# Kernel optimization log

Hardware: AMD Instinct MI355X
Metric: run time of the kernel (lower is better)

## Reference

```python
import jax, jax.numpy as jnp
import numpy as np

N, E, B = 20000, 60000, 800
H = 64          # node_out_feats
EOUT = 64       # edge_out_feats
D = H + EOUT    # set2set input dim = 128
NT = 138        # n_tasks


def _forward(node_feats, edge_feats, fp_vector, src, dst, gid,
             Wn, bn, We1, be1, We2, be2, Wres, Wgx, bgx, Wgh, bgh,
             Wep, bep,
             Wlx0, Wlh0, bl0, Wlx1, Wlh1, bl1, Wlx2, Wlh2, bl2,
             Wfp, bfp, bn_g, bn_b, bn_m, bn_v,
             Wf1, bf1, Wf2, bf2, Wp, bp):
    # ---- CustomMPNNGNN (dgllife MPNNGNN: proj + NNConv(edge-net) + GRU) ----
    h = jax.nn.relu(node_feats @ Wn + bn)                       # [N,64]
    We = jax.nn.relu(edge_feats @ We1 + be1) @ We2 + be2        # [E,4096]
    We = We.reshape(-1, H, H)                                   # [E,64,64] per-edge weight
    hs = h                                                      # GRU hidden state
    for _ in range(3):
        msg = jnp.einsum('ei,eio->eo', h[src], We)              # edge gather + matvec
        agg = jax.ops.segment_sum(msg, dst, num_segments=N)     # scatter-add to dst
        m = jax.nn.relu(agg + h @ Wres)                         # residual root weight
        gx = m @ Wgx + bgx
        gh = hs @ Wgh + bgh
        xr, xz, xn = jnp.split(gx, 3, axis=-1)
        hr, hz, hn = jnp.split(gh, 3, axis=-1)
        r = jax.nn.sigmoid(xr + hr)
        z = jax.nn.sigmoid(xz + hz)
        n = jnp.tanh(xn + r * hn)
        hs = (1.0 - z) * n + z * hs
        h = hs
    # ---- _internal_readout: gather src node emb + projected edge emb, segment-sum at dst ----
    e_emb = jax.nn.relu(edge_feats @ Wep + bep)                 # [E,64]
    src_msg = jnp.concatenate([h[src], e_emb], axis=1)          # [E,128]
    feat = jax.ops.segment_sum(src_msg, dst, num_segments=N)    # [N,128]
    # ---- Set2Set (3-layer LSTM hidden 128, 6 iterations) ----
    q_star = jnp.zeros((B, 2 * D), feat.dtype)
    hc = [(jnp.zeros((B, D), feat.dtype), jnp.zeros((B, D), feat.dtype)) for _ in range(3)]
    lstm = [(Wlx0, Wlh0, bl0), (Wlx1, Wlh1, bl1), (Wlx2, Wlh2, bl2)]
    for _ in range(6):
        x = q_star
        new_hc = []
        for (Wx, Wh, b), (hl, cl) in zip(lstm, hc):
            g = x @ Wx + hl @ Wh + b                            # [B,512] gates i,f,g,o
            gi, gf, gg, go = jnp.split(g, 4, axis=-1)
            cl = jax.nn.sigmoid(gf) * cl + jax.nn.sigmoid(gi) * jnp.tanh(gg)
            hl = jax.nn.sigmoid(go) * jnp.tanh(cl)
            new_hc.append((hl, cl))
            x = hl
        hc = new_hc
        q = x                                                   # [B,128]
        e = jnp.sum(feat * q[gid], axis=-1)                     # [N]
        emax = jax.ops.segment_max(e, gid, num_segments=B)
        a = jnp.exp(e - emax[gid])
        denom = jax.ops.segment_sum(a, gid, num_segments=B)
        alpha = a / (denom[gid] + 1e-9)
        r = jax.ops.segment_sum(alpha[:, None] * feat, gid, num_segments=B)  # [B,128]
        q_star = jnp.concatenate([q, r], axis=1)                # [B,256]
    # ---- Fingerprint encoder: Linear + BatchNorm1d(eval) + ReLU ----
    fp = fp_vector @ Wfp + bfp
    fp = jax.nn.relu((fp - bn_m) * bn_g * jax.lax.rsqrt(bn_v + 1e-5) + bn_b)  # [B,128]
    # ---- combined FFN (384 -> 300 -> 256) + prediction head ----
    comb = jnp.concatenate([q_star, fp], axis=1)                # [B,384]
    emb = jax.nn.relu(comb @ Wf1 + bf1) @ Wf2 + bf2             # [B,256]
    out = jax.nn.relu(emb) @ Wp + bp                            # [B,138]
    return out


def setup_inputs() -> dict:
    key = jax.random.key(0)
    ks = iter(jax.random.split(key, 64))
    def nrm(shape, s):
        return jax.random.normal(next(ks), shape, jnp.float32) * s
    inp = {}
    inp['node_feats'] = jax.random.normal(next(ks), (N, 134), jnp.float32)
    inp['edge_feats'] = jax.random.uniform(next(ks), (E, 6), jnp.float32)
    inp['fp_vector'] = jax.random.uniform(next(ks), (B, 1024), jnp.float32)
    inp['src'] = jax.random.randint(next(ks), (E,), 0, N)
    inp['dst'] = jax.random.randint(next(ks), (E,), 0, N)
    inp['gid'] = jnp.sort(jax.random.randint(next(ks), (N,), 0, B))
    # MPNN params
    inp['Wn'] = nrm((134, H), 0.08); inp['bn'] = jnp.zeros((H,), jnp.float32)
    inp['We1'] = nrm((6, 128), 0.2); inp['be1'] = jnp.zeros((128,), jnp.float32)
    inp['We2'] = nrm((128, H * H), 0.05); inp['be2'] = jnp.zeros((H * H,), jnp.float32)
    inp['Wres'] = nrm((H, H), 0.1)
    inp['Wgx'] = nrm((H, 3 * H), 0.1); inp['bgx'] = jnp.zeros((3 * H,), jnp.float32)
    inp['Wgh'] = nrm((H, 3 * H), 0.1); inp['bgh'] = jnp.zeros((3 * H,), jnp.float32)
    # edge projection for readout
    inp['Wep'] = nrm((6, EOUT), 0.2); inp['bep'] = jnp.zeros((EOUT,), jnp.float32)
    # Set2Set LSTM (layer0 input 2D=256, layers 1-2 input D=128, hidden D=128)
    inp['Wlx0'] = nrm((2 * D, 4 * D), 0.06); inp['Wlh0'] = nrm((D, 4 * D), 0.06); inp['bl0'] = jnp.zeros((4 * D,), jnp.float32)
    inp['Wlx1'] = nrm((D, 4 * D), 0.06); inp['Wlh1'] = nrm((D, 4 * D), 0.06); inp['bl1'] = jnp.zeros((4 * D,), jnp.float32)
    inp['Wlx2'] = nrm((D, 4 * D), 0.06); inp['Wlh2'] = nrm((D, 4 * D), 0.06); inp['bl2'] = jnp.zeros((4 * D,), jnp.float32)
    # fingerprint encoder
    inp['Wfp'] = nrm((1024, 128), 0.03); inp['bfp'] = jnp.zeros((128,), jnp.float32)
    inp['bn_g'] = jnp.ones((128,), jnp.float32); inp['bn_b'] = jnp.zeros((128,), jnp.float32)
    inp['bn_m'] = jnp.zeros((128,), jnp.float32); inp['bn_v'] = jnp.ones((128,), jnp.float32)
    # combined FFN + prediction head
    inp['Wf1'] = nrm((2 * D + 128, 300), 0.06); inp['bf1'] = jnp.zeros((300,), jnp.float32)
    inp['Wf2'] = nrm((300, 256), 0.06); inp['bf2'] = jnp.zeros((256,), jnp.float32)
    inp['Wp'] = nrm((256, NT), 0.06); inp['bp'] = jnp.zeros((NT,), jnp.float32)
    return inp


def reference(node_feats, edge_feats, fp_vector, src, dst, gid,
              Wn, bn, We1, be1, We2, be2, Wres, Wgx, bgx, Wgh, bgh,
              Wep, bep,
              Wlx0, Wlh0, bl0, Wlx1, Wlh1, bl1, Wlx2, Wlh2, bl2,
              Wfp, bfp, bn_g, bn_b, bn_m, bn_v,
              Wf1, bf1, Wf2, bf2, Wp, bp):
    return _forward(node_feats, edge_feats, fp_vector, src, dst, gid,
                    Wn, bn, We1, be1, We2, be2, Wres, Wgx, bgx, Wgh, bgh,
                    Wep, bep,
                    Wlx0, Wlh0, bl0, Wlx1, Wlh1, bl1, Wlx2, Wlh2, bl2,
                    Wfp, bfp, bn_g, bn_b, bn_m, bn_v,
                    Wf1, bf1, Wf2, bf2, Wp, bp)
```

## Files before the change

kernel.cpp:

```cpp
#include <hip/hip_runtime.h>

typedef short short8 __attribute__((ext_vector_type(8)));
typedef float f32x4  __attribute__((ext_vector_type(4)));

#define NN 20000
#define NE 60000
#define NB 800
#define NTASK 138
#define EB 128

#define O_WX0 0
#define O_WH0 131072
#define O_WX1 196608
#define O_WH1 262144
#define O_WX2 327680
#define O_WH2 393216
#define O_WF1 458752
#define O_WF2 573952
#define O_WP  650752
#define NWB   686080

static __device__ __forceinline__ float sigm(float x) { return 1.f / (1.f + expf(-x)); }

static __device__ __forceinline__ unsigned short f2bf(float x) {
    unsigned u = __float_as_uint(x);
    unsigned r = (u + 0x7fffu + ((u >> 16) & 1u)) >> 16;
    return (unsigned short)r;
}
static __device__ __forceinline__ float bf2f(unsigned short b) {
    return __uint_as_float(((unsigned)b) << 16);
}

__global__ void kpre(float* __restrict__ zbase, int nz4,
                     const float* __restrict__ We2, const float* __restrict__ be2,
                     unsigned short* __restrict__ thi,
                     const int* __restrict__ gid, int* __restrict__ seg,
                     const float* __restrict__ fpv, const float* __restrict__ Wfp,
                     const float* __restrict__ bfpv,
                     const float* __restrict__ bng, const float* __restrict__ bnb,
                     const float* __restrict__ bnm, const float* __restrict__ bnv,
                     float* __restrict__ fpb,
                     const float* __restrict__ nf, const float* __restrict__ Wn,
                     const float* __restrict__ bn, float* __restrict__ hf,
                     unsigned short* __restrict__ hb,
                     const float* __restrict__ Wlx0, const float* __restrict__ Wlh0,
                     const float* __restrict__ Wlx1, const float* __restrict__ Wlh1,
                     const float* __restrict__ Wlx2, const float* __restrict__ Wlh2,
                     const float* __restrict__ Wf1, const float* __restrict__ Wf2,
                     const float* __restrict__ Wp, unsigned short* __restrict__ wb,
                     int B0, int B1, int B2, int B3, int B4) {
    __shared__ float st[64 * 65];
    __shared__ float sNF[16 * 134];
    __shared__ float sred[128];
    const int bid = blockIdx.x, tid = threadIdx.x;
    if (bid < B0) {
        long base = (long)bid * 2048 + tid;
        #pragma unroll
        for (int r = 0; r < 8; ++r) {
            long i = base + r * 256;
            if (i < nz4) reinterpret_cast<f32x4*>(zbase)[i] = f32x4{0.f, 0.f, 0.f, 0.f};
        }
    } else if (bid < B1) {
        int c = bid - B0;
        const float* srcp = (c < 128) ? We2 + (long)c * 4096 : be2;
        for (int idx = tid; idx < 4096; idx += 256) {
            int o = idx & 63, i = idx >> 6;
            st[o * 65 + i] = srcp[idx];
        }
        __syncthreads();
        for (int idx = tid; idx < 4096; idx += 256) {
            int i = idx & 63, o = idx >> 6;
            thi[(long)c * 4096 + idx] = f2bf(st[o * 65 + i]);
        }
    } else if (bid < B2) {
        int b = (bid - B1) * 256 + tid;
        if (b <= NB) {
            int lo = 0, hi = NN;
            while (lo < hi) { int mid = (lo + hi) >> 1; if (gid[mid] < b) lo = mid + 1; else hi = mid; }
            seg[b] = lo;
        }
    } else if (bid < B3) {
        int g = bid - B2;
        int u = tid & 127, half = tid >> 7;
        float acc = half ? 0.f : bfpv[u];
        const float* fr = fpv + (long)g * 1024 + half * 512;
        const float* wr = Wfp + (long)half * 512 * 128;
        for (int k = 0; k < 512; ++k) acc += fr[k] * wr[k * 128 + u];
        if (half) sred[u] = acc;
        __syncthreads();
        if (!half) {
            acc += sred[u];
            float sc = bng[u] / sqrtf(bnv[u] + 1e-5f);
            fpb[(long)g * 128 + u] = fmaxf((acc - bnm[u]) * sc + bnb[u], 0.f);
        }
    } else if (bid < B4) {
        int n0 = (bid - B3) * 16;
        const float* nfb = nf + (long)n0 * 134;
        for (int i = tid; i < 16 * 134; i += 256) sNF[i] = nfb[i];
        __syncthreads();
        int u = tid & 63, jg = tid >> 6;
        float a[4];
        float bv = bn[u];
        #pragma unroll
        for (int jj = 0; jj < 4; ++jj) a[jj] = bv;
        for (int k = 0; k < 134; ++k) {
            float w = Wn[k * 64 + u];
            #pragma unroll
            for (int jj = 0; jj < 4; ++jj) a[jj] += sNF[(jg * 4 + jj) * 134 + k] * w;
        }
        #pragma unroll
        for (int jj = 0; jj < 4; ++jj) {
            long o = (long)(n0 + jg * 4 + jj) * 64 + u;
            float v = fmaxf(a[jj], 0.f);
            hf[o] = v;
            hb[o] = f2bf(v);
        }
    } else {
        int t0 = (bid - B4) * 2048 + tid;
        #pragma unroll
        for (int r = 0; r < 8; ++r) {
            int i = t0 + r * 256;
            if (i >= NWB) break;
            float v;
            if (i < O_WF1) {
                const float* srcp; int base;
                if (i < O_WH0)      { srcp = Wlx0; base = O_WX0; }
                else if (i < O_WX1) { srcp = Wlh0; base = O_WH0; }
                else if (i < O_WH1) { srcp = Wlx1; base = O_WX1; }
                else if (i < O_WX2) { srcp = Wlh1; base = O_WH1; }
                else if (i < O_WH2) { srcp = Wlx2; base = O_WX2; }
                else                { srcp = Wlh2; base = O_WH2; }
                int il = i - base;
                int kb = il >> 12, g = (il >> 3) & 511, kk = il & 7;
                v = srcp[(kb * 8 + kk) * 512 + g];
            }
            else if (i < O_WF2) v = Wf1[i - O_WF1];
            else if (i < O_WP)  v = Wf2[i - O_WF2];
            else                v = Wp[i - O_WP];
            wb[i] = f2bf(v);
        }
    }
}

__global__ __launch_bounds__(256) void keinsum(
    const unsigned short* __restrict__ hb,
    const float* __restrict__ hf, const float* __restrict__ Wres,
    const float* __restrict__ ef, const float* __restrict__ We1, const float* __restrict__ be1,
    const unsigned short* __restrict__ thi,
    const int* __restrict__ src, const int* __restrict__ dst,
    float* __restrict__ agg) {
    __shared__ __align__(16) unsigned short sB[3 * 64 * 72];
    __shared__ __align__(16) float sX[3 * EB];
    __shared__ float sEF[6 * EB];
    const int bid = blockIdx.x, tid = threadIdx.x;
    if (bid >= 469) {
        int t = (bid - 469) * 256 + tid;
        int u = t & 63;
        int n0 = (t >> 6) * 8;
        if (n0 >= NN) return;
        float a[8] = {0.f, 0.f, 0.f, 0.f, 0.f, 0.f, 0.f, 0.f};
        for (int k = 0; k < 64; ++k) {
            float w = Wres[k * 64 + u];
            #pragma unroll
            for (int j = 0; j < 8; ++j) a[j] += hf[(long)(n0 + j) * 64 + k] * w;
        }
        #pragma unroll
        for (int j = 0; j < 8; ++j) atomicAdd(&agg[(long)(n0 + j) * 64 + u], a[j]);
        return;
    }
    const int lane = tid & 63, wave = tid >> 6;
    const int m = lane & 15, q = lane >> 4;
    const int eb = bid * EB;
    const int ew = (wave >> 1) * 64;
    const int e0 = eb + ew;
    const int nt0 = (wave & 1) * 2;
    const int c0 = 0, c1 = 129;

    for (int i = tid; i < 6 * EB; i += 256) {
        int e = i / 6, k = i % 6;
        int ee = eb + e; if (ee >= NE) ee = NE - 1;
        sEF[k * EB + e] = ef[(long)ee * 6 + k];
    }

    short8 ahi[4][2];
    #pragma unroll
    for (int eg = 0; eg < 4; ++eg) {
        int em = e0 + eg * 16 + m; if (em >= NE) em = NE - 1;
        int sn = src[em];
        ahi[eg][0] = *reinterpret_cast<const short8*>(hb + (long)sn * 64 + q * 8);
        ahi[eg][1] = *reinterpret_cast<const short8*>(hb + (long)sn * 64 + 32 + q * 8);
    }
    float msg[4][2][4];
    #pragma unroll
    for (int eg = 0; eg < 4; ++eg)
        #pragma unroll
        for (int nt = 0; nt < 2; ++nt)
            #pragma unroll
            for (int r = 0; r < 4; ++r) msg[eg][nt][r] = 0.f;

    short8 rB[2][2];
    auto GLOAD = [&](int c, int setv) {
        const unsigned short* bb = thi + (long)c * 4096;
        #pragma unroll
        for (int it = 0; it < 2; ++it) {
            int u = tid + it * 256;
            rB[setv][it] = *reinterpret_cast<const short8*>(bb + u * 8);
        }
    };
    auto DSW = [&](int buf, int setv, int c) {
        unsigned short* base = &sB[buf * 4608];
        #pragma unroll
        for (int it = 0; it < 2; ++it) {
            int u = tid + it * 256;
            *reinterpret_cast<short8*>(&base[(u >> 3) * 72 + (u & 7) * 8]) = rB[setv][it];
        }
        if (tid < EB) {
            float xv = 1.f;
            if (c < 128) {
                float a = be1[c];
                #pragma unroll
                for (int k = 0; k < 6; ++k) a += sEF[k * EB + tid] * We1[k * 128 + c];
                xv = fmaxf(a, 0.f);
            }
            sX[buf * EB + tid] = xv;
        }
    };
    auto CMP = [&](int buf) {
        const unsigned short* base = &sB[buf * 4608];
        f32x4 xw[4];
        #pragma unroll
        for (int eg = 0; eg < 4; ++eg)
            xw[eg] = *reinterpret_cast<const f32x4*>(&sX[buf * EB + ew + eg * 16 + q * 4]);
        short8 b0[2], b1[2];
        #pragma unroll
        for (int nt = 0; nt < 2; ++nt) {
            const unsigned short* rp = &base[((nt0 + nt) * 16 + m) * 72 + q * 8];
            b0[nt] = *reinterpret_cast<const short8*>(rp);
            b1[nt] = *reinterpret_cast<const short8*>(rp + 32);
        }
        #pragma unroll
        for (int eg = 0; eg < 4; ++eg)
            #pragma unroll
            for (int nt = 0; nt < 2; ++nt) {
                f32x4 z = {0.f, 0.f, 0.f, 0.f};
                z = __builtin_amdgcn_mfma_f32_16x16x32_bf16(ahi[eg][0], b0[nt], z, 0, 0, 0);
                z = __builtin_amdgcn_mfma_f32_16x16x32_bf16(ahi[eg][1], b1[nt], z, 0, 0, 0);
                #pragma unroll
                for (int r = 0; r < 4; ++r) msg[eg][nt][r] += xw[eg][r] * z[r];
            }
    };

    GLOAD(c0, 0);
    GLOAD(c0 + 1, 1);
    __syncthreads();
    DSW(0, 0, c0);
    int c = c0;
    for (; c + 1 < c1; c += 2) {
        int s = (c - c0) % 3;
        if (c + 2 < c1) GLOAD(c + 2, 0);
        __syncthreads();
        DSW((s + 1) % 3, 1, c + 1);
        CMP(s);
        if (c + 3 < c1) GLOAD(c + 3, 1);
        __syncthreads();
        if (c + 2 < c1) DSW((s + 2) % 3, 0, c + 2);
        CMP((s + 1) % 3);
    }
    if (c < c1) { __syncthreads(); CMP((c - c0) % 3); }

    #pragma unroll
    for (int eg = 0; eg < 4; ++eg)
        #pragma unroll
        for (int r = 0; r < 4; ++r) {
            int e = e0 + eg * 16 + q * 4 + r;
            if (e < NE) {
                int d = dst[e];
                #pragma unroll
                for (int nt = 0; nt < 2; ++nt)
                    atomicAdd(&agg[(long)d * 64 + (nt0 + nt) * 16 + m], msg[eg][nt][r]);
            }
        }
}

__global__ void kgruz(const float* __restrict__ agg, const float* __restrict__ h,
                      const float* __restrict__ Wgx, const float* __restrict__ bgx,
                      const float* __restrict__ Wgh, const float* __restrict__ bgh,
                      float* __restrict__ hof, unsigned short* __restrict__ hb,
                      float* __restrict__ aggN) {
    const int bid = blockIdx.x, tid = threadIdx.x;
    if (bid >= 625) {
        long base = (long)(bid - 625) * 2048 + tid;
        #pragma unroll
        for (int r = 0; r < 8; ++r) {
            long i = base + r * 256;
            if (i < 320000) reinterpret_cast<f32x4*>(aggN)[i] = f32x4{0.f, 0.f, 0.f, 0.f};
        }
        return;
    }
    __shared__ float sA[2048], sH[2048];
    const int n0 = bid * 32;
    const float* ab = agg + (long)n0 * 64;
    const float* hrow = h + (long)n0 * 64;
    for (int i = tid; i < 2048; i += 256) { sA[i] = ab[i]; sH[i] = hrow[i]; }
    __syncthreads();
    const int u = tid & 63, jg = tid >> 6;
    float xr[8], xz[8], xn[8], hr[8], hz[8], hn[8];
    float b0 = bgx[u], b1 = bgx[64 + u], b2 = bgx[128 + u];
    float d0 = bgh[u], d1 = bgh[64 + u], d2 = bgh[128 + u];
    #pragma unroll
    for (int j = 0; j < 8; ++j) {
        xr[j] = b0; xz[j] = b1; xn[j] = b2;
        hr[j] = d0; hz[j] = d1; hn[j] = d2;
    }
    for (int k = 0; k < 64; ++k) {
        float w0 = Wgx[k * 192 + u], w1 = Wgx[k * 192 + 64 + u], w2 = Wgx[k * 192 + 128 + u];
        float v0 = Wgh[k * 192 + u], v1 = Wgh[k * 192 + 64 + u], v2 = Wgh[k * 192 + 128 + u];
        #pragma unroll
        for (int j = 0; j < 8; ++j) {
            int n = jg * 8 + j;
            float mk = fmaxf(sA[n * 64 + k], 0.f);
            float hk = sH[n * 64 + k];
            xr[j] += mk * w0; xz[j] += mk * w1; xn[j] += mk * w2;
            hr[j] += hk * v0; hz[j] += hk * v1; hn[j] += hk * v2;
        }
    }
    #pragma unroll
    for (int j = 0; j < 8; ++j) {
        int n = jg * 8 + j;
        float rg = sigm(xr[j] + hr[j]);
        float zg = sigm(xz[j] + hz[j]);
        float ng = tanhf(xn[j] + rg * hn[j]);
        long o = (long)(n0 + n) * 64 + u;
        float hv = (1.f - zg) * ng + zg * sH[n * 64 + u];
        hof[o] = hv;
        hb[o] = f2bf(hv);
    }
}

__global__ void kreadout(const float* __restrict__ h,
                         const float* __restrict__ ef, const float* __restrict__ Wep,
                         const float* __restrict__ bep,
                         const int* __restrict__ src, const int* __restrict__ dst,
                         float* __restrict__ feat) {
    int t = blockIdx.x * blockDim.x + threadIdx.x;
    if (t >= NE * 128) return;
    int e = t >> 7, j = t & 127;
    float v;
    if (j < 64) {
        v = h[(long)src[e] * 64 + j];
    } else {
        int o = j - 64;
        v = bep[o];
        #pragma unroll
        for (int k = 0; k < 6; ++k) v += ef[(long)e * 6 + k] * Wep[k * 64 + o];
        v = fmaxf(v, 0.f);
    }
    atomicAdd(&feat[(long)dst[e] * 128 + j], v);
}

__global__ __launch_bounds__(512) void klstmattn(
    const float* __restrict__ qstar_in, float* __restrict__ qstar_out,
    const float* __restrict__ feat, const int* __restrict__ seg,
    float* __restrict__ esg,
    const unsigned short* __restrict__ wb,
    const float* __restrict__ bl0, const float* __restrict__ bl1, const float* __restrict__ bl2,
    const float* __restrict__ h0i, const float* __restrict__ c0i, float* __restrict__ h0o, float* __restrict__ c0o,
    const float* __restrict__ h1i, const float* __restrict__ c1i, float* __restrict__ h1o, float* __restrict__ c1o,
    const float* __restrict__ h2i, const float* __restrict__ c2i, float* __restrict__ h2o, float* __restrict__ c2o,
    const float* __restrict__ fpb,
    const float* __restrict__ bf1, const float* __restrict__ bf2, const float* __restrict__ bp,
    float* __restrict__ out, int do_head) {
    __shared__ float sXH[2][256];
    __shared__ float sHin[2][128];
    __shared__ float sG[2][512];
    __shared__ float sE[2][512];
    __shared__ float sH2[2][128];
    __shared__ float sR[2][2][128];
    __shared__ float sred[2][4];
    __shared__ float s1b[2][300];
    __shared__ float s2[2][256];
    const int tid = threadIdx.x;
    const int b0g = blockIdx.x * 2;
    const unsigned short* Wx[3] = {wb + O_WX0, wb + O_WX1, wb + O_WX2};
    const unsigned short* Wh[3] = {wb + O_WH0, wb + O_WH1, wb + O_WH2};
    const float* bl[3] = {bl0, bl1, bl2};
    const float* hin[3] = {h0i, h1i, h2i};
    const float* cin[3] = {c0i, c1i, c2i};
    float* hout[3] = {h0o, h1o, h2o};
    float* cout[3] = {c0o, c1o, c2o};

    {
        int b = tid >> 8, u = tid & 255;
        sXH[b][u] = qstar_in[(long)(b0g + b) * 256 + u];
        if (tid < 256) {
            int bb = tid >> 7, uu = tid & 127;
            sHin[bb][uu] = h0i[(long)(b0g + bb) * 128 + uu];
        }
    }
    __syncthreads();

    for (int l = 0; l < 3; ++l) {
        const int Kx = l ? 128 : 256;
        const int g = tid;
        const unsigned short* wxp = Wx[l];
        const unsigned short* whp = Wh[l];
        float bv = bl[l][g];
        float a0 = bv, a1 = bv, a0b = 0.f, a1b = 0.f;
        #pragma unroll 2
        for (int kb = 0; kb < (Kx >> 3); ++kb) {
            short8 wv = *reinterpret_cast<const short8*>(wxp + ((kb << 9) + g) * 8);
            const f32x4* xp0 = reinterpret_cast<const f32x4*>(&sXH[0][kb << 3]);
            const f32x4* xp1 = reinterpret_cast<const f32x4*>(&sXH[1][kb << 3]);
            f32x4 xa0 = xp0[0], xb0 = xp0[1];
            f32x4 xa1 = xp1[0], xb1 = xp1[1];
            #pragma unroll
            for (int kk = 0; kk < 4; ++kk) {
                float w0 = bf2f((unsigned short)wv[kk]);
                float w1 = bf2f((unsigned short)wv[kk + 4]);
                a0  += xa0[kk] * w0;  a1  += xa1[kk] * w0;
                a0b += xb0[kk] * w1;  a1b += xb1[kk] * w1;
            }
        }
        #pragma unroll 2
        for (int kb = 0; kb < 16; ++kb) {
            short8 wv = *reinterpret_cast<const short8*>(whp + ((kb << 9) + g) * 8);
            const f32x4* hp0 = reinterpret_cast<const f32x4*>(&sHin[0][kb << 3]);
            const f32x4* hp1 = reinterpret_cast<const f32x4*>(&sHin[1][kb << 3]);
            f32x4 ha0 = hp0[0], hb0 = hp0[1];
            f32x4 ha1 = hp1[0], hb1 = hp1[1];
            #pragma unroll
            for (int kk = 0; kk < 4; ++kk) {
                float w0 = bf2f((unsigned short)wv[kk]);
                float w1 = bf2f((unsigned short)wv[kk + 4]);
                a0  += ha0[kk] * w0;  a1  += ha1[kk] * w0;
                a0b += hb0[kk] * w1;  a1b += hb1[kk] * w1;
            }
        }
        sG[0][g] = a0 + a0b;
        sG[1][g] = a1 + a1b;
        __syncthreads();
        if (tid < 256) {
            int b = tid >> 7, u = tid & 127;
            float gi = sG[b][u], gf = sG[b][128 + u], gg = sG[b][256 + u], go = sG[b][384 + u];
            long idx = (long)(b0g + b) * 128 + u;
            float c_ = sigm(gf) * cin[l][idx] + sigm(gi) * tanhf(gg);
            float h_ = sigm(go) * tanhf(c_);
            cout[l][idx] = c_;
            hout[l][idx] = h_;
            sXH[b][u] = h_;
            if (l == 2) sH2[b][u] = h_;
        } else if (l < 2) {
            int t2 = tid - 256;
            int b = t2 >> 7, u = t2 & 127;
            sHin[b][u] = hin[l + 1][(long)(b0g + b) * 128 + u];
        }
        __syncthreads();
    }

    const int group = tid >> 8;
    const int t = tid & 255;
    const int s0 = seg[b0g + group], s1 = seg[b0g + group + 1], len = s1 - s0;
    const int wv = t >> 6, lane = t & 63;
    for (int idx = wv; idx < len; idx += 4) {
        long n = s0 + idx;
        float p = feat[n * 128 + lane] * sH2[group][lane]
                + feat[n * 128 + 64 + lane] * sH2[group][64 + lane];
        for (int off = 32; off; off >>= 1) p += __shfl_down(p, off, 64);
        if (lane == 0) { if (idx < 512) sE[group][idx] = p; else esg[n] = p; }
    }
    __syncthreads();
    auto ev = [&](int i) { return i < 512 ? sE[group][i] : esg[s0 + i]; };
    float lm = -1e30f;
    for (int i = t; i < len; i += 256) lm = fmaxf(lm, ev(i));
    for (int off = 32; off; off >>= 1) lm = fmaxf(lm, __shfl_down(lm, off, 64));
    if (lane == 0) sred[group][wv] = lm;
    __syncthreads();
    float mx = fmaxf(fmaxf(sred[group][0], sred[group][1]),
                     fmaxf(sred[group][2], sred[group][3]));
    __syncthreads();
    float ls = 0.f;
    for (int i = t; i < len; i += 256) {
        float e_ = expf(ev(i) - mx);
        if (i < 512) sE[group][i] = e_; else esg[s0 + i] = e_;
        ls += e_;
    }
    for (int off = 32; off; off >>= 1) ls += __shfl_down(ls, off, 64);
    if (lane == 0) sred[group][wv] = ls;
    __syncthreads();
    float inv = 1.f / (sred[group][0] + sred[group][1] + sred[group][2] + sred[group][3] + 1e-9f);
    const int j = t & 127, half = t >> 7;
    float racc = 0.f;
    for (int i = half; i < len; i += 2)
        racc += ev(i) * feat[(long)(s0 + i) * 128 + j];
    sR[group][half][j] = racc;
    __syncthreads();
    float rr = (sR[group][0][j] + sR[group][1][j]) * inv;
    if (half == 0) {
        qstar_out[(long)(b0g + group) * 256 + j] = sH2[group][j];
        qstar_out[(long)(b0g + group) * 256 + 128 + j] = rr;
    }

    if (!do_head) return;
    __syncthreads();
    if (half == 0) {
        sE[group][j] = sH2[group][j];
        sE[group][128 + j] = rr;
    } else {
        sE[group][256 + j] = fpb[(long)(b0g + group) * 128 + j];
    }
    __syncthreads();
    const unsigned short* Wf1b = wb + O_WF1;
    const unsigned short* Wf2b = wb + O_WF2;
    const unsigned short* Wpb  = wb + O_WP;
    for (int task = tid; task < 600; task += 512) {
        int g = task / 300, u = task % 300;
        float acc = bf1[u];
        for (int k = 0; k < 384; ++k) acc += sE[g][k] * bf2f(Wf1b[k * 300 + u]);
        s1b[g][u] = fmaxf(acc, 0.f);
    }
    __syncthreads();
    for (int task = tid; task < 512; task += 512) {
        int g = task >> 8, u = task & 255;
        float acc = bf2[u];
        for (int k = 0; k < 300; ++k) acc += s1b[g][k] * bf2f(Wf2b[k * 256 + u]);
        s2[g][u] = fmaxf(acc, 0.f);
    }
    __syncthreads();
    for (int task = tid; task < 2 * NTASK; task += 512) {
        int g = task / NTASK, u = task % NTASK;
        float acc = bp[u];
        for (int k = 0; k < 256; ++k) acc += s2[g][k] * bf2f(Wpb[k * NTASK + u]);
        out[(long)(b0g + g) * NTASK + u] = acc;
    }
}

extern "C" void kernel_launch(void* const* d_in, const int* in_sizes, int n_in,
                              void* d_out, int out_size, void* d_ws, size_t ws_size,
                              hipStream_t stream) {
    auto fp_ = [&](int i) { return (const float*)d_in[i]; };
    auto ip_ = [&](int i) { return (const int*)d_in[i]; };
    const float *nf = fp_(0), *ef = fp_(1), *fpv = fp_(2);
    const int *src = ip_(3), *dst = ip_(4), *gid = ip_(5);
    const float *Wn = fp_(6), *bn = fp_(7), *We1 = fp_(8), *be1 = fp_(9);
    const float *We2 = fp_(10), *be2 = fp_(11), *Wres = fp_(12);
    const float *Wgx = fp_(13), *bgx = fp_(14), *Wgh = fp_(15), *bgh = fp_(16);
    const float *Wep = fp_(17), *bep = fp_(18);
    const float *Wlx0 = fp_(19), *Wlh0 = fp_(20), *bl0 = fp_(21);
    const float *Wlx1 = fp_(22), *Wlh1 = fp_(23), *bl1 = fp_(24);
    const float *Wlx2 = fp_(25), *Wlh2 = fp_(26), *bl2 = fp_(27);
    const float *Wfp = fp_(28), *bfpv = fp_(29);
    const float *bng = fp_(30), *bnb = fp_(31), *bnm = fp_(32), *bnv = fp_(33);
    const float *Wf1 = fp_(34), *bf1 = fp_(35), *Wf2 = fp_(36), *bf2 = fp_(37);
    const float *Wp = fp_(38), *bp = fp_(39);

    char* w = (char*)d_ws;
    auto alloc = [&](size_t bytes) -> char* {
        char* p = w; w += (bytes + 255) & ~(size_t)255; return p;
    };
    float* hA = (float*)alloc((size_t)NN * 64 * 4);
    float* hB = (float*)alloc((size_t)NN * 64 * 4);
    unsigned short* hbA = (unsigned short*)alloc((size_t)NN * 64 * 2);
    unsigned short* hbB = (unsigned short*)alloc((size_t)NN * 64 * 2);
    unsigned short* we2thi = (unsigned short*)alloc((size_t)129 * 4096 * 2);
    unsigned short* wbf = (unsigned short*)alloc((size_t)NWB * 2);
    float* aggB = (float*)alloc((size_t)NN * 64 * 4);
    char* zstart = w;
    float* aggA  = (float*)alloc((size_t)NN * 64 * 4);
    float* feat  = (float*)alloc((size_t)NN * 128 * 4);
    float* qstarA = (float*)alloc((size_t)NB * 256 * 4);
    float* qstarB = (float*)alloc((size_t)NB * 256 * 4);
    float* lstmb = (float*)alloc((size_t)12 * NB * 128 * 4);
    size_t zfloats = (size_t)(w - zstart) / 4;
    float* es   = (float*)alloc((size_t)NN * 4);
    int*   seg  = (int*)alloc((size_t)(NB + 1) * 4);
    float* fpb  = (float*)alloc((size_t)NB * 128 * 4);

    float *hl[3][2], *cl[3][2];
    for (int l = 0; l < 3; ++l)
        for (int a = 0; a < 2; ++a) {
            hl[l][a] = lstmb + ((size_t)(l * 4 + a * 2 + 0)) * NB * 128;
            cl[l][a] = lstmb + ((size_t)(l * 4 + a * 2 + 1)) * NB * 128;
        }

    int nz4 = (int)(zfloats / 4);
    int zb  = (nz4 + 2047) / 2048;
    int B0 = zb;
    int B1 = B0 + 129;
    int B2 = B1 + 4;
    int B3 = B2 + NB;
    int B4 = B3 + 1250;
    int B5 = B4 + (NWB + 2047) / 2048;
    kpre<<<B5, 256, 0, stream>>>((float*)zstart, nz4, We2, be2, we2thi, gid, seg,
                                 fpv, Wfp, bfpv, bng, bnb, bnm, bnv, fpb,
                                 nf, Wn, bn, hA, hbA,
                                 Wlx0, Wlh0, Wlx1, Wlh1, Wlx2, Wlh2, Wf1, Wf2, Wp, wbf,
                                 B0, B1, B2, B3, B4);

    float* hf[2] = {hA, hB};
    unsigned short* hb[2] = {hbA, hbB};
    float* aggbuf[2] = {aggA, aggB};
    int cur = 0;
    for (int it = 0; it < 3; ++it) {
        float* agg  = aggbuf[it & 1];
        float* aggN = aggbuf[1 - (it & 1)];
        keinsum<<<469 + 625, 256, 0, stream>>>(hb[cur], hf[cur], Wres,
                                               ef, We1, be1, we2thi, src, dst, agg);
        kgruz<<<625 + 157, 256, 0, stream>>>(agg, hf[cur], Wgx, bgx, Wgh, bgh,
                                             hf[1 - cur], hb[1 - cur], aggN);
        cur = 1 - cur;
    }
    kreadout<<<(NE * 128 + 255) / 256, 256, 0, stream>>>(hf[cur], ef, Wep, bep, src, dst, feat);

    float* qs[2] = {qstarA, qstarB};
    for (int t = 0; t < 6; ++t) {
        int a = t & 1;
        klstmattn<<<NB / 2, 512, 0, stream>>>(qs[a], qs[1 - a], feat, seg, es,
            wbf, bl0, bl1, bl2,
            hl[0][a], cl[0][a], hl[0][1 - a], cl[0][1 - a],
            hl[1][a], cl[1][a], hl[1][1 - a], cl[1][1 - a],
            hl[2][a], cl[2][a], hl[2][1 - a], cl[2][1 - a],
            fpb, bf1, bf2, bp, (float*)d_out, (t == 5) ? 1 : 0);
    }
}
```

Baseline: 893.7 us.

## Precompute edge hidden activations once and stream B fragments directly from global

The first edge-MLP layer relu(ef@We1+be1) is now computed once in the prologue kernel and stored transposed as a [128, EPAD] fp32 buffer. Before, each of the three message-passing iterations recomputed it per chunk. The einsum kernel also drops its LDS triple-buffered staging and barriers, loading bf16 weight fragments and x values straight from global memory into registers with two-deep register double buffering. This removes redundant arithmetic and synchronisation. In exchange it adds about 30 MB of extra global reads per iteration and depends on the L2 cache serving the shared weight fragments.

```diff
diff --git a/kernel.cpp b/kernel.cpp
--- a/kernel.cpp
+++ b/kernel.cpp
@@ -8,6 +8,7 @@
 #define NB 800
 #define NTASK 138
 #define EB 128
+#define EPAD 60032
 
 #define O_WX0 0
 #define O_WH0 131072
@@ -43,15 +44,19 @@
                      const float* __restrict__ nf, const float* __restrict__ Wn,
                      const float* __restrict__ bn, float* __restrict__ hf,
                      unsigned short* __restrict__ hb,
+                     const float* __restrict__ ef, const float* __restrict__ We1,
+                     const float* __restrict__ be1, float* __restrict__ xt,
                      const float* __restrict__ Wlx0, const float* __restrict__ Wlh0,
                      const float* __restrict__ Wlx1, const float* __restrict__ Wlh1,
                      const float* __restrict__ Wlx2, const float* __restrict__ Wlh2,
                      const float* __restrict__ Wf1, const float* __restrict__ Wf2,
                      const float* __restrict__ Wp, unsigned short* __restrict__ wb,
-                     int B0, int B1, int B2, int B3, int B4) {
+                     int B0, int B1, int B2, int B3, int B4, int B5) {
     __shared__ float st[64 * 65];
     __shared__ float sNF[16 * 134];
     __shared__ float sred[128];
+    __shared__ float sW[6 * 128];
+    __shared__ float sbv[128];
     const int bid = blockIdx.x, tid = threadIdx.x;
     if (bid < B0) {
         long base = (long)bid * 2048 + tid;
@@ -115,8 +120,25 @@
             hf[o] = v;
             hb[o] = f2bf(v);
         }
+    } else if (bid < B5) {
+        for (int i = tid; i < 768; i += 256) sW[i] = We1[i];
+        if (tid < 128) sbv[tid] = be1[tid];
+        __syncthreads();
+        int e = (bid - B4) * 256 + tid;
+        if (e < NE) {
+            float e0 = ef[(long)e * 6 + 0], e1 = ef[(long)e * 6 + 1], e2 = ef[(long)e * 6 + 2];
+            float e3 = ef[(long)e * 6 + 3], e4 = ef[(long)e * 6 + 4], e5 = ef[(long)e * 6 + 5];
+            for (int c = 0; c < 128; ++c) {
+                float a = sbv[c];
+                a += e0 * sW[c];       a += e1 * sW[128 + c]; a += e2 * sW[256 + c];
+                a += e3 * sW[384 + c]; a += e4 * sW[512 + c]; a += e5 * sW[640 + c];
+                xt[(long)c * EPAD + e] = fmaxf(a, 0.f);
+            }
+        } else if (e < EPAD) {
+            for (int c = 0; c < 128; ++c) xt[(long)c * EPAD + e] = 0.f;
+        }
     } else {
-        int t0 = (bid - B4) * 2048 + tid;
+        int t0 = (bid - B5) * 2048 + tid;
         #pragma unroll
         for (int r = 0; r < 8; ++r) {
             int i = t0 + r * 256;
@@ -145,13 +167,10 @@
 __global__ __launch_bounds__(256) void keinsum(
     const unsigned short* __restrict__ hb,
     const float* __restrict__ hf, const float* __restrict__ Wres,
-    const float* __restrict__ ef, const float* __restrict__ We1, const float* __restrict__ be1,
+    const float* __restrict__ xt,
     const unsigned short* __restrict__ thi,
     const int* __restrict__ src, const int* __restrict__ dst,
     float* __restrict__ agg) {
-    __shared__ __align__(16) unsigned short sB[3 * 64 * 72];
-    __shared__ __align__(16) float sX[3 * EB];
-    __shared__ float sEF[6 * EB];
     const int bid = blockIdx.x, tid = threadIdx.x;
     if (bid >= 469) {
         int t = (bid - 469) * 256 + tid;
@@ -174,13 +193,6 @@
     const int ew = (wave >> 1) * 64;
     const int e0 = eb + ew;
     const int nt0 = (wave & 1) * 2;
-    const int c0 = 0, c1 = 129;
-
-    for (int i = tid; i < 6 * EB; i += 256) {
-        int e = i / 6, k = i % 6;
-        int ee = eb + e; if (ee >= NE) ee = NE - 1;
-        sEF[k * EB + e] = ef[(long)ee * 6 + k];
-    }
 
     short8 ahi[4][2];
     #pragma unroll
@@ -190,83 +202,58 @@
         ahi[eg][0] = *reinterpret_cast<const short8*>(hb + (long)sn * 64 + q * 8);
         ahi[eg][1] = *reinterpret_cast<const short8*>(hb + (long)sn * 64 + 32 + q * 8);
     }
-    float msg[4][2][4];
+
+    f32x4 msg[4][2];
     #pragma unroll
     for (int eg = 0; eg < 4; ++eg)
         #pragma unroll
-        for (int nt = 0; nt < 2; ++nt)
+        for (int nt = 0; nt < 2; ++nt) msg[eg][nt] = f32x4{0.f, 0.f, 0.f, 0.f};
+
+    const unsigned short* bfrag = thi + (nt0 * 16 + m) * 64 + q * 8;
+    const float* xbase = xt + e0 + q * 4;
+
+    short8 b0A[2], b1A[2], b0B[2], b1B[2];
+    f32x4 xA[4], xB[4];
+
+    auto LD = [&](int c, short8 (&cb0)[2], short8 (&cb1)[2], f32x4 (&cx)[4]) {
+        const unsigned short* bp = bfrag + (long)c * 4096;
+        #pragma unroll
+        for (int nt = 0; nt < 2; ++nt) {
+            cb0[nt] = *reinterpret_cast<const short8*>(bp + nt * 1024);
+            cb1[nt] = *reinterpret_cast<const short8*>(bp + nt * 1024 + 32);
+        }
+        if (c < 128) {
+            const float* xp = xbase + (long)c * EPAD;
             #pragma unroll
-            for (int r = 0; r < 4; ++r) msg[eg][nt][r] = 0.f;
-
-    short8 rB[2][2];
-    auto GLOAD = [&](int c, int setv) {
-        const unsigned short* bb = thi + (long)c * 4096;
-        #pragma unroll
-        for (int it = 0; it < 2; ++it) {
-            int u = tid + it * 256;
-            rB[setv][it] = *reinterpret_cast<const short8*>(bb + u * 8);
+            for (int eg = 0; eg < 4; ++eg)
+                cx[eg] = *reinterpret_cast<const f32x4*>(xp + eg * 16);
+        } else {
+            #pragma unroll
+            for (int eg = 0; eg < 4; ++eg) cx[eg] = f32x4{1.f, 1.f, 1.f, 1.f};
         }
     };
-    auto DSW = [&](int buf, int setv, int c) {
-        unsigned short* base = &sB[buf * 4608];
-        #pragma unroll
-        for (int it = 0; it < 2; ++it) {
-            int u = tid + it * 256;
-            *reinterpret_cast<short8*>(&base[(u >> 3) * 72 + (u & 7) * 8]) = rB[setv][it];
-        }
-        if (tid < EB) {
-            float xv = 1.f;
-            if (c < 128) {
-                float a = be1[c];
-                #pragma unroll
-                for (int k = 0; k < 6; ++k) a += sEF[k * EB + tid] * We1[k * 128 + c];
-                xv = fmaxf(a, 0.f);
-            }
-            sX[buf * EB + tid] = xv;
-        }
-    };
-    auto CMP = [&](int buf) {
-        const unsigned short* base = &sB[buf * 4608];
-        f32x4 xw[4];
-        #pragma unroll
-        for (int eg = 0; eg < 4; ++eg)
-            xw[eg] = *reinterpret_cast<const f32x4*>(&sX[buf * EB + ew + eg * 16 + q * 4]);
-        short8 b0[2], b1[2];
-        #pragma unroll
-        for (int nt = 0; nt < 2; ++nt) {
-            const unsigned short* rp = &base[((nt0 + nt) * 16 + m) * 72 + q * 8];
-            b0[nt] = *reinterpret_cast<const short8*>(rp);
-            b1[nt] = *reinterpret_cast<const short8*>(rp + 32);
-        }
+    auto CMP = [&](short8 (&cb0)[2], short8 (&cb1)[2], f32x4 (&cx)[4]) {
         #pragma unroll
         for (int eg = 0; eg < 4; ++eg)
             #pragma unroll
             for (int nt = 0; nt < 2; ++nt) {
                 f32x4 z = {0.f, 0.f, 0.f, 0.f};
-                z = __builtin_amdgcn_mfma_f32_16x16x32_bf16(ahi[eg][0], b0[nt], z, 0, 0, 0);
-                z = __builtin_amdgcn_mfma_f32_16x16x32_bf16(ahi[eg][1], b1[nt], z, 0, 0, 0);
-                #pragma unroll
-                for (int r = 0; r < 4; ++r) msg[eg][nt][r] += xw[eg][r] * z[r];
+                z = __builtin_amdgcn_mfma_f32_16x16x32_bf16(ahi[eg][0], cb0[nt], z, 0, 0, 0);
+                z = __builtin_amdgcn_mfma_f32_16x16x32_bf16(ahi[eg][1], cb1[nt], z, 0, 0, 0);
+                msg[eg][nt] += cx[eg] * z;
             }
     };
 
-    GLOAD(c0, 0);
-    GLOAD(c0 + 1, 1);
-    __syncthreads();
-    DSW(0, 0, c0);
-    int c = c0;
-    for (; c + 1 < c1; c += 2) {
-        int s = (c - c0) % 3;
-        if (c + 2 < c1) GLOAD(c + 2, 0);
-        __syncthreads();
-        DSW((s + 1) % 3, 1, c + 1);
-        CMP(s);
-        if (c + 3 < c1) GLOAD(c + 3, 1);
-        __syncthreads();
-        if (c + 2 < c1) DSW((s + 2) % 3, 0, c + 2);
-        CMP((s + 1) % 3);
-    }
-    if (c < c1) { __syncthreads(); CMP((c - c0) % 3); }
+    LD(0, b0A, b1A, xA);
+    LD(1, b0B, b1B, xB);
+    int c = 0;
+    for (; c + 1 < 129; c += 2) {
+        CMP(b0A, b1A, xA);
+        if (c + 2 < 129) LD(c + 2, b0A, b1A, xA);
+        CMP(b0B, b1B, xB);
+        if (c + 3 < 129) LD(c + 3, b0B, b1B, xB);
+    }
+    if (c < 129) CMP(b0A, b1A, xA);
 
     #pragma unroll
     for (int eg = 0; eg < 4; ++eg)
@@ -574,6 +561,7 @@
     float* es   = (float*)alloc((size_t)NN * 4);
     int*   seg  = (int*)alloc((size_t)(NB + 1) * 4);
     float* fpb  = (float*)alloc((size_t)NB * 128 * 4);
+    float* xt   = (float*)alloc((size_t)128 * EPAD * 4);
 
     float *hl[3][2], *cl[3][2];
     for (int l = 0; l < 3; ++l)
@@ -589,12 +577,14 @@
     int B2 = B1 + 4;
     int B3 = B2 + NB;
     int B4 = B3 + 1250;
-    int B5 = B4 + (NWB + 2047) / 2048;
-    kpre<<<B5, 256, 0, stream>>>((float*)zstart, nz4, We2, be2, we2thi, gid, seg,
+    int B5 = B4 + 235;
+    int B6 = B5 + (NWB + 2047) / 2048;
+    kpre<<<B6, 256, 0, stream>>>((float*)zstart, nz4, We2, be2, we2thi, gid, seg,
                                  fpv, Wfp, bfpv, bng, bnb, bnm, bnv, fpb,
                                  nf, Wn, bn, hA, hbA,
+                                 ef, We1, be1, xt,
                                  Wlx0, Wlh0, Wlx1, Wlh1, Wlx2, Wlh2, Wf1, Wf2, Wp, wbf,
-                                 B0, B1, B2, B3, B4);
+                                 B0, B1, B2, B3, B4, B5);
 
     float* hf[2] = {hA, hB};
     unsigned short* hb[2] = {hbA, hbB};
@@ -604,7 +594,7 @@
         float* agg  = aggbuf[it & 1];
         float* aggN = aggbuf[1 - (it & 1)];
         keinsum<<<469 + 625, 256, 0, stream>>>(hb[cur], hf[cur], Wres,
-                                               ef, We1, be1, we2thi, src, dst, agg);
+                                               xt, we2thi, src, dst, agg);
         kgruz<<<625 + 157, 256, 0, stream>>>(agg, hf[cur], Wgx, bgx, Wgh, bgh,
                                              hf[1 - cur], hb[1 - cur], aggN);
         cur = 1 - cur;
```

Result: slower. 1.098 ms (+22.9%).
